# Optimization experiments

Measured on AMD Instinct MI355X. Metric: run time of the kernel, lower is better.

Reference implementation:

```python
import jax, jax.numpy as jnp
import numpy as np

N_NODES = 100000
N_EDGES = 800000
N_GRAPHS = 256
IN_C = 96
HID = 96
OUT_C = 16


def setup_inputs() -> dict:
    key = jax.random.key(0)
    ks = jax.random.split(key, 10)
    x = jax.random.normal(ks[0], (N_NODES, IN_C), dtype=jnp.float32)
    edge_index = jax.random.randint(ks[1], (2, N_EDGES), 0, N_NODES, dtype=jnp.int64)
    batch = jnp.sort(jax.random.randint(ks[2], (N_NODES,), 0, N_GRAPHS, dtype=jnp.int64))
    def glorot(k, fan_in, fan_out):
        s = np.sqrt(6.0 / (fan_in + fan_out)).astype(np.float32)
        return jax.random.uniform(k, (fan_in, fan_out), minval=-s, maxval=s, dtype=jnp.float32)
    W1 = glorot(ks[3], IN_C, HID)
    W2 = glorot(ks[4], HID, HID)
    W3 = glorot(ks[5], HID, HID)
    Wlin = glorot(ks[6], HID, OUT_C)
    b1 = jnp.zeros((HID,), dtype=jnp.float32)
    b2 = jnp.zeros((HID,), dtype=jnp.float32)
    b3 = jnp.zeros((HID,), dtype=jnp.float32)
    return {"x": x, "edge_index": edge_index, "batch": batch,
            "W1": W1, "b1": b1, "W2": W2, "b2": b2, "W3": W3, "b3": b3, "Wlin": Wlin}


def _gcn_conv(x, W, b, src, dst):
    # PyG GCNConv(normalize=True): add self-loops, deg includes self-loop,
    # norm_ij = deg_i^{-1/2} * deg_j^{-1/2}; linear (no bias) then scatter-add; bias after.
    n = x.shape[0]
    deg = jnp.zeros((n,), dtype=x.dtype).at[dst].add(1.0) + 1.0  # +1 self-loop
    dinv = jax.lax.rsqrt(deg)
    h = x @ W                                   # [N, H]
    coef = dinv[src] * dinv[dst]                # [E]
    msg = h[src] * coef[:, None]                # [E, H] gather
    agg = jax.ops.segment_sum(msg, dst, num_segments=n)  # scatter-add
    agg = agg + h * (dinv * dinv)[:, None]      # self-loop contribution
    return agg + b


def reference(x, edge_index, batch, W1, b1, W2, b2, W3, b3, Wlin):
    src, dst = edge_index[0], edge_index[1]
    h = jax.nn.relu(_gcn_conv(x, W1, b1, src, dst))
    h = jax.nn.relu(_gcn_conv(h, W2, b2, src, dst))
    h = _gcn_conv(h, W3, b3, src, dst)
    # global mean pool over graphs
    sums = jax.ops.segment_sum(h, batch, num_segments=N_GRAPHS)
    counts = jax.ops.segment_sum(jnp.ones((h.shape[0],), dtype=h.dtype), batch, num_segments=N_GRAPHS)
    pooled = sums / jnp.maximum(counts, 1.0)[:, None]
    return pooled @ Wlin
```

## Files before the change

### kernel.cpp

```cpp
#include <hip/hip_runtime.h>

#define NN 100000
#define NE 800000
#define NG 256
#define CH 96
#define OC 16
#define NBLK 391
#define TM 128

typedef __attribute__((ext_vector_type(8))) short bf16x8;
typedef __attribute__((ext_vector_type(4))) float f32x4;

__device__ __forceinline__ unsigned short f2bf(float x) {
    unsigned u = __float_as_uint(x);
    return (unsigned short)((u + 0x7fffu + ((u >> 16) & 1u)) >> 16);
}
__device__ __forceinline__ float bf2f(unsigned short h) {
    return __uint_as_float(((unsigned)h) << 16);
}
__device__ __forceinline__ void split8(const float4 a, const float4 b,
                                       bf16x8& hi, bf16x8& lo) {
    float v[8] = {a.x, a.y, a.z, a.w, b.x, b.y, b.z, b.w};
#pragma unroll
    for (int j = 0; j < 8; j++) {
        unsigned short h = f2bf(v[j]);
        hi[j] = (short)h;
        lo[j] = (short)f2bf(v[j] - bf2f(h));
    }
}
__device__ __forceinline__ float4 us4_to_f4(ushort4 u) {
    return make_float4(bf2f(u.x), bf2f(u.y), bf2f(u.z), bf2f(u.w));
}

__global__ __launch_bounds__(256) void k_hist(const int* __restrict__ dst,
                                              int* __restrict__ cnt,
                                              int* __restrict__ slot) {
    int e = blockIdx.x * 256 + threadIdx.x;
    slot[e] = atomicAdd(&cnt[dst[e]], 1);
}

__global__ __launch_bounds__(256) void k_offsets(const int* __restrict__ cnt,
                                                 int* __restrict__ gtot,
                                                 int* __restrict__ off,
                                                 float* __restrict__ dinv,
                                                 const int* __restrict__ batch,
                                                 int* __restrict__ goff) {
    int i = blockIdx.x * 256 + threadIdx.x;
    if (i >= NN) return;
    int c = cnt[i];
    off[i] = atomicAdd(gtot, c);
    dinv[i] = rsqrtf((float)c + 1.0f);
    int b = batch[i];
    int bp = (i > 0) ? batch[i - 1] : -1;
    for (int g = bp + 1; g <= b; g++) goff[g] = i;
    if (i == NN - 1)
        for (int g = b + 1; g <= NG; g++) goff[g] = NN;
}

__global__ __launch_bounds__(256) void k_build(const int* __restrict__ src,
                                               const int* __restrict__ dst,
                                               const int* __restrict__ off,
                                               const int* __restrict__ slot,
                                               const float* __restrict__ dinv,
                                               float2* __restrict__ packed) {
    int e = blockIdx.x * 256 + threadIdx.x;
    int s = src[e];
    int d = dst[e];
    packed[off[d] + slot[e]] = make_float2(__int_as_float(s), dinv[s] * dinv[d]);
    if (blockIdx.x == 0 && threadIdx.x < 8)
        packed[NE + threadIdx.x] = make_float2(__int_as_float(0), 0.0f);
}

__global__ __launch_bounds__(256) void k_prep(const float* __restrict__ W1,
                                              const float* __restrict__ W2,
                                              const float* __restrict__ W3,
                                              unsigned short* __restrict__ WH,
                                              unsigned short* __restrict__ WL) {
    int id = blockIdx.x * 256 + threadIdx.x;
    if (id >= 3 * CH * CH) return;
    int w = id / (CH * CH);
    int r = id - w * CH * CH;
    int k = r / CH;
    int n = r - k * CH;
    const float* Ws = (w == 0) ? W1 : (w == 1) ? W2 : W3;
    float v = Ws[k * CH + n];
    unsigned short h = f2bf(v);
    WH[w * CH * CH + n * CH + k] = h;
    WL[w * CH * CH + n * CH + k] = f2bf(v - bf2f(h));
}

__global__ __launch_bounds__(256) void k_gemm96(const float* __restrict__ X,
                                                const unsigned short* __restrict__ WH,
                                                const unsigned short* __restrict__ WL,
                                                unsigned short* __restrict__ H) {
    __shared__ __align__(16) unsigned short WsH[CH * CH];
    __shared__ __align__(16) unsigned short WsL[CH * CH];

    const int tid = threadIdx.x;
    const int n0 = blockIdx.x * TM;

    {
        const uint4* sH = reinterpret_cast<const uint4*>(WH);
        const uint4* sL = reinterpret_cast<const uint4*>(WL);
        uint4* dH = reinterpret_cast<uint4*>(WsH);
        uint4* dL = reinterpret_cast<uint4*>(WsL);
        for (int i = tid; i < CH * CH / 8; i += 256) {
            dH[i] = sH[i];
            dL[i] = sL[i];
        }
    }
    __syncthreads();

    const int lane = tid & 63;
    const int wave = tid >> 6;
    const int lrow = lane & 15;
    const int quad = lane >> 4;

    const float4* X4 = reinterpret_cast<const float4*>(X);

    f32x4 acc[2][6];
#pragma unroll
    for (int rt = 0; rt < 2; rt++)
#pragma unroll
        for (int ct = 0; ct < 6; ct++) acc[rt][ct] = (f32x4){0.f, 0.f, 0.f, 0.f};

    int arow[2];
#pragma unroll
    for (int rt = 0; rt < 2; rt++)
        arow[rt] = min(n0 + (wave * 2 + rt) * 16 + lrow, NN - 1);

#pragma unroll
    for (int kc = 0; kc < 3; kc++) {
        bf16x8 ahi[2], alo[2];
#pragma unroll
        for (int rt = 0; rt < 2; rt++) {
            int fo = (arow[rt] * CH + kc * 32 + quad * 8) >> 2;
            split8(X4[fo], X4[fo + 1], ahi[rt], alo[rt]);
        }
#pragma unroll
        for (int ct = 0; ct < 6; ct++) {
            int bo = (ct * 16 + lrow) * CH + kc * 32 + quad * 8;
            bf16x8 bhi = *reinterpret_cast<const bf16x8*>(&WsH[bo]);
            bf16x8 blo = *reinterpret_cast<const bf16x8*>(&WsL[bo]);
#pragma unroll
            for (int rt = 0; rt < 2; rt++) {
                acc[rt][ct] = __builtin_amdgcn_mfma_f32_16x16x32_bf16(
                    alo[rt], bhi, acc[rt][ct], 0, 0, 0);
                acc[rt][ct] = __builtin_amdgcn_mfma_f32_16x16x32_bf16(
                    ahi[rt], blo, acc[rt][ct], 0, 0, 0);
                acc[rt][ct] = __builtin_amdgcn_mfma_f32_16x16x32_bf16(
                    ahi[rt], bhi, acc[rt][ct], 0, 0, 0);
            }
        }
    }

#pragma unroll
    for (int rt = 0; rt < 2; rt++) {
        int rbase = n0 + (wave * 2 + rt) * 16 + quad * 4;
#pragma unroll
        for (int ct = 0; ct < 6; ct++) {
            int col = ct * 16 + lrow;
#pragma unroll
            for (int r = 0; r < 4; r++) {
                int row = rbase + r;
                if (row < NN) H[(size_t)row * CH + col] = f2bf(acc[rt][ct][r]);
            }
        }
    }
}

template <bool RELU>
__global__ __launch_bounds__(256) void k_aggregate(const int* __restrict__ off,
                                                   const int* __restrict__ cnt,
                                                   const float2* __restrict__ packed,
                                                   const float* __restrict__ dinv,
                                                   const float* __restrict__ bias,
                                                   const unsigned short* __restrict__ H,
                                                   float* __restrict__ B) {
    int idx = blockIdx.x * 256 + threadIdx.x;
    int n = idx / 24;
    int c4 = idx - n * 24;
    int e0 = off[n];
    int e1 = e0 + cnt[n];

    const ushort4* H4 = reinterpret_cast<const ushort4*>(H);
    float di = dinv[n];
    float d2 = di * di;
    float4 h = us4_to_f4(H4[(size_t)n * 24 + c4]);
    float4 bb = reinterpret_cast<const float4*>(bias)[c4];
    float4 acc = make_float4(h.x * d2 + bb.x, h.y * d2 + bb.y,
                             h.z * d2 + bb.z, h.w * d2 + bb.w);

    for (int e = e0; e < e1; e += 4) {
        float2 p0 = packed[e + 0];
        float2 p1 = packed[e + 1];
        float2 p2 = packed[e + 2];
        float2 p3 = packed[e + 3];
        float c0 = p0.y;
        float c1 = (e + 1 < e1) ? p1.y : 0.0f;
        float c2 = (e + 2 < e1) ? p2.y : 0.0f;
        float c3 = (e + 3 < e1) ? p3.y : 0.0f;
        float4 v0 = us4_to_f4(H4[(size_t)__float_as_int(p0.x) * 24 + c4]);
        float4 v1 = us4_to_f4(H4[(size_t)__float_as_int(p1.x) * 24 + c4]);
        float4 v2 = us4_to_f4(H4[(size_t)__float_as_int(p2.x) * 24 + c4]);
        float4 v3 = us4_to_f4(H4[(size_t)__float_as_int(p3.x) * 24 + c4]);
        acc.x += v0.x * c0 + v1.x * c1 + v2.x * c2 + v3.x * c3;
        acc.y += v0.y * c0 + v1.y * c1 + v2.y * c2 + v3.y * c3;
        acc.z += v0.z * c0 + v1.z * c1 + v2.z * c2 + v3.z * c3;
        acc.w += v0.w * c0 + v1.w * c1 + v2.w * c2 + v3.w * c3;
    }
    if (RELU) {
        acc.x = fmaxf(acc.x, 0.0f); acc.y = fmaxf(acc.y, 0.0f);
        acc.z = fmaxf(acc.z, 0.0f); acc.w = fmaxf(acc.w, 0.0f);
    }
    reinterpret_cast<float4*>(B)[(size_t)n * 24 + c4] = acc;
}


__global__ __launch_bounds__(384) void k_pool_linear(const int* __restrict__ goff,
                                                     const float* __restrict__ B,
                                                     const float* __restrict__ Wlin,
                                                     float* __restrict__ out) {
    __shared__ float4 sh[16][24];
    __shared__ float pooled[CH];
    int g = blockIdx.x;
    int t = threadIdx.x;
    int nl = t / 24;
    int c4 = t - nl * 24;
    int s = goff[g];
    int e = goff[g + 1];

    float4 acc = make_float4(0.f, 0.f, 0.f, 0.f);
    const float4* B4 = reinterpret_cast<const float4*>(B);
    for (int n = s + nl; n < e; n += 16) {
        float4 v = B4[(size_t)n * 24 + c4];
        acc.x += v.x; acc.y += v.y; acc.z += v.z; acc.w += v.w;
    }
    sh[nl][c4] = acc;
    __syncthreads();

    if (t < 24) {
        float4 r = make_float4(0.f, 0.f, 0.f, 0.f);
#pragma unroll
        for (int j = 0; j < 16; j++) {
            float4 v = sh[j][t];
            r.x += v.x; r.y += v.y; r.z += v.z; r.w += v.w;
        }
        float inv = 1.0f / fmaxf((float)(e - s), 1.0f);
        pooled[t * 4 + 0] = r.x * inv;
        pooled[t * 4 + 1] = r.y * inv;
        pooled[t * 4 + 2] = r.z * inv;
        pooled[t * 4 + 3] = r.w * inv;
    }
    __syncthreads();

    if (t < OC) {
        float a = 0.0f;
#pragma unroll 8
        for (int k = 0; k < CH; k++) a += pooled[k] * Wlin[k * OC + t];
        out[g * OC + t] = a;
    }
}

extern "C" void kernel_launch(void* const* d_in, const int* in_sizes, int n_in,
                              void* d_out, int out_size, void* d_ws, size_t ws_size,
                              hipStream_t stream) {
    const float* x = (const float*)d_in[0];
    const int* ei = (const int*)d_in[1];
    const int* src = ei;
    const int* dst = ei + NE;
    const int* batch = (const int*)d_in[2];
    const float* W1 = (const float*)d_in[3];
    const float* b1 = (const float*)d_in[4];
    const float* W2 = (const float*)d_in[5];
    const float* b2 = (const float*)d_in[6];
    const float* W3 = (const float*)d_in[7];
    const float* b3 = (const float*)d_in[8];
    const float* Wlin = (const float*)d_in[9];
    float* out = (float*)d_out;

    char* ws = (char*)d_ws;
    unsigned short* Ha = (unsigned short*)ws;  ws += (size_t)NN * CH * 2;
    unsigned short* Hb = (unsigned short*)ws;  ws += (size_t)NN * CH * 2;
    float* B = (float*)ws;          ws += (size_t)NN * CH * 4;
    float2* packed = (float2*)ws;   ws += (size_t)(NE + 8) * 8;
    unsigned short* WH = (unsigned short*)ws;  ws += 3 * CH * CH * 2;
    unsigned short* WL = (unsigned short*)ws;  ws += 3 * CH * CH * 2;
    float* dinv = (float*)ws;       ws += NN * 4;
    int* off = (int*)ws;            ws += NN * 4;
    int* goff = (int*)ws;           ws += 272 * 4;
    int* cnt = (int*)ws;            ws += (NN + 4) * 4;
    int* gtot = cnt + NN;
    int* slot = (int*)B;

    hipMemsetAsync(cnt, 0, (NN + 4) * 4, stream);
    k_hist<<<NE / 256, 256, 0, stream>>>(dst, cnt, slot);
    k_offsets<<<NBLK, 256, 0, stream>>>(cnt, gtot, off, dinv, batch, goff);
    k_build<<<NE / 256, 256, 0, stream>>>(src, dst, off, slot, dinv, packed);
    k_prep<<<(3 * CH * CH + 255) / 256, 256, 0, stream>>>(W1, W2, W3, WH, WL);

    const int gblk = (NN + TM - 1) / TM;

    k_gemm96<<<gblk, 256, 0, stream>>>(x, WH, WL, Ha);
    k_aggregate<true><<<NN * 24 / 256, 256, 0, stream>>>(off, cnt, packed, dinv, b1, Ha, B);

    k_gemm96<<<gblk, 256, 0, stream>>>(B, WH + CH * CH, WL + CH * CH, Hb);
    k_aggregate<true><<<NN * 24 / 256, 256, 0, stream>>>(off, cnt, packed, dinv, b2, Hb, B);

    k_gemm96<<<gblk, 256, 0, stream>>>(B, WH + 2 * CH * CH, WL + 2 * CH * CH, Ha);
    k_aggregate<false><<<NN * 24 / 256, 256, 0, stream>>>(off, cnt, packed, dinv, b3, Ha, B);

    k_pool_linear<<<NG, 384, 0, stream>>>(goff, B, Wlin, out);
}
```

Measured before the change: 331.3 us.

## Store intermediate layer activations in bf16 and fold weight prep into histogram

```diff
diff --git a/kernel.cpp b/kernel.cpp
--- a/kernel.cpp
+++ b/kernel.cpp
@@ -34,9 +34,25 @@
 
 __global__ __launch_bounds__(256) void k_hist(const int* __restrict__ dst,
                                               int* __restrict__ cnt,
-                                              int* __restrict__ slot) {
+                                              int* __restrict__ slot,
+                                              const float* __restrict__ W1,
+                                              const float* __restrict__ W2,
+                                              const float* __restrict__ W3,
+                                              unsigned short* __restrict__ WH,
+                                              unsigned short* __restrict__ WL) {
     int e = blockIdx.x * 256 + threadIdx.x;
     slot[e] = atomicAdd(&cnt[dst[e]], 1);
+    if (e < 3 * CH * CH) {
+        int w = e / (CH * CH);
+        int r = e - w * (CH * CH);
+        int k = r / CH;
+        int n = r - k * CH;
+        const float* Ws = (w == 0) ? W1 : (w == 1) ? W2 : W3;
+        float v = Ws[k * CH + n];
+        unsigned short h = f2bf(v);
+        WH[w * CH * CH + n * CH + k] = h;
+        WL[w * CH * CH + n * CH + k] = f2bf(v - bf2f(h));
+    }
 }
 
 __global__ __launch_bounds__(256) void k_offsets(const int* __restrict__ cnt,
@@ -67,32 +83,12 @@
     int s = src[e];
     int d = dst[e];
     packed[off[d] + slot[e]] = make_float2(__int_as_float(s), dinv[s] * dinv[d]);
-    if (blockIdx.x == 0 && threadIdx.x < 8)
-        packed[NE + threadIdx.x] = make_float2(__int_as_float(0), 0.0f);
-}
-
-__global__ __launch_bounds__(256) void k_prep(const float* __restrict__ W1,
-                                              const float* __restrict__ W2,
-                                              const float* __restrict__ W3,
-                                              unsigned short* __restrict__ WH,
-                                              unsigned short* __restrict__ WL) {
-    int id = blockIdx.x * 256 + threadIdx.x;
-    if (id >= 3 * CH * CH) return;
-    int w = id / (CH * CH);
-    int r = id - w * CH * CH;
-    int k = r / CH;
-    int n = r - k * CH;
-    const float* Ws = (w == 0) ? W1 : (w == 1) ? W2 : W3;
-    float v = Ws[k * CH + n];
-    unsigned short h = f2bf(v);
-    WH[w * CH * CH + n * CH + k] = h;
-    WL[w * CH * CH + n * CH + k] = f2bf(v - bf2f(h));
-}
-
-__global__ __launch_bounds__(256) void k_gemm96(const float* __restrict__ X,
-                                                const unsigned short* __restrict__ WH,
-                                                const unsigned short* __restrict__ WL,
-                                                unsigned short* __restrict__ H) {
+}
+
+__global__ __launch_bounds__(256) void k_gemm_f32(const float* __restrict__ X,
+                                                  const unsigned short* __restrict__ WH,
+                                                  const unsigned short* __restrict__ WL,
+                                                  unsigned short* __restrict__ H) {
     __shared__ __align__(16) unsigned short WsH[CH * CH];
     __shared__ __align__(16) unsigned short WsL[CH * CH];
 
@@ -169,14 +165,89 @@
     }
 }
 
-template <bool RELU>
+__global__ __launch_bounds__(256) void k_gemm_bf16(const unsigned short* __restrict__ X,
+                                                   const unsigned short* __restrict__ WH,
+                                                   const unsigned short* __restrict__ WL,
+                                                   unsigned short* __restrict__ H) {
+    __shared__ __align__(16) unsigned short WsH[CH * CH];
+    __shared__ __align__(16) unsigned short WsL[CH * CH];
+
+    const int tid = threadIdx.x;
+    const int n0 = blockIdx.x * TM;
+
+    {
+        const uint4* sH = reinterpret_cast<const uint4*>(WH);
+        const uint4* sL = reinterpret_cast<const uint4*>(WL);
+        uint4* dH = reinterpret_cast<uint4*>(WsH);
+        uint4* dL = reinterpret_cast<uint4*>(WsL);
+        for (int i = tid; i < CH * CH / 8; i += 256) {
+            dH[i] = sH[i];
+            dL[i] = sL[i];
+        }
+    }
+    __syncthreads();
+
+    const int lane = tid & 63;
+    const int wave = tid >> 6;
+    const int lrow = lane & 15;
+    const int quad = lane >> 4;
+
+    f32x4 acc[2][6];
+#pragma unroll
+    for (int rt = 0; rt < 2; rt++)
+#pragma unroll
+        for (int ct = 0; ct < 6; ct++) acc[rt][ct] = (f32x4){0.f, 0.f, 0.f, 0.f};
+
+    int arow[2];
+#pragma unroll
+    for (int rt = 0; rt < 2; rt++)
+        arow[rt] = min(n0 + (wave * 2 + rt) * 16 + lrow, NN - 1);
+
+#pragma unroll
+    for (int kc = 0; kc < 3; kc++) {
+        bf16x8 ahi[2];
+#pragma unroll
+        for (int rt = 0; rt < 2; rt++)
+            ahi[rt] = *reinterpret_cast<const bf16x8*>(
+                &X[(size_t)arow[rt] * CH + kc * 32 + quad * 8]);
+#pragma unroll
+        for (int ct = 0; ct < 6; ct++) {
+            int bo = (ct * 16 + lrow) * CH + kc * 32 + quad * 8;
+            bf16x8 bhi = *reinterpret_cast<const bf16x8*>(&WsH[bo]);
+            bf16x8 blo = *reinterpret_cast<const bf16x8*>(&WsL[bo]);
+#pragma unroll
+            for (int rt = 0; rt < 2; rt++) {
+                acc[rt][ct] = __builtin_amdgcn_mfma_f32_16x16x32_bf16(
+                    ahi[rt], blo, acc[rt][ct], 0, 0, 0);
+                acc[rt][ct] = __builtin_amdgcn_mfma_f32_16x16x32_bf16(
+                    ahi[rt], bhi, acc[rt][ct], 0, 0, 0);
+            }
+        }
+    }
+
+#pragma unroll
+    for (int rt = 0; rt < 2; rt++) {
+        int rbase = n0 + (wave * 2 + rt) * 16 + quad * 4;
+#pragma unroll
+        for (int ct = 0; ct < 6; ct++) {
+            int col = ct * 16 + lrow;
+#pragma unroll
+            for (int r = 0; r < 4; r++) {
+                int row = rbase + r;
+                if (row < NN) H[(size_t)row * CH + col] = f2bf(acc[rt][ct][r]);
+            }
+        }
+    }
+}
+
+template <bool RELU, bool B16OUT>
 __global__ __launch_bounds__(256) void k_aggregate(const int* __restrict__ off,
                                                    const int* __restrict__ cnt,
                                                    const float2* __restrict__ packed,
                                                    const float* __restrict__ dinv,
                                                    const float* __restrict__ bias,
                                                    const unsigned short* __restrict__ H,
-                                                   float* __restrict__ B) {
+                                                   void* __restrict__ Bout) {
     int idx = blockIdx.x * 256 + threadIdx.x;
     int n = idx / 24;
     int c4 = idx - n * 24;
@@ -191,31 +262,39 @@
     float4 acc = make_float4(h.x * d2 + bb.x, h.y * d2 + bb.y,
                              h.z * d2 + bb.z, h.w * d2 + bb.w);
 
-    for (int e = e0; e < e1; e += 4) {
+    int e = e0;
+    for (; e + 4 <= e1; e += 4) {
         float2 p0 = packed[e + 0];
         float2 p1 = packed[e + 1];
         float2 p2 = packed[e + 2];
         float2 p3 = packed[e + 3];
-        float c0 = p0.y;
-        float c1 = (e + 1 < e1) ? p1.y : 0.0f;
-        float c2 = (e + 2 < e1) ? p2.y : 0.0f;
-        float c3 = (e + 3 < e1) ? p3.y : 0.0f;
         float4 v0 = us4_to_f4(H4[(size_t)__float_as_int(p0.x) * 24 + c4]);
         float4 v1 = us4_to_f4(H4[(size_t)__float_as_int(p1.x) * 24 + c4]);
         float4 v2 = us4_to_f4(H4[(size_t)__float_as_int(p2.x) * 24 + c4]);
         float4 v3 = us4_to_f4(H4[(size_t)__float_as_int(p3.x) * 24 + c4]);
-        acc.x += v0.x * c0 + v1.x * c1 + v2.x * c2 + v3.x * c3;
-        acc.y += v0.y * c0 + v1.y * c1 + v2.y * c2 + v3.y * c3;
-        acc.z += v0.z * c0 + v1.z * c1 + v2.z * c2 + v3.z * c3;
-        acc.w += v0.w * c0 + v1.w * c1 + v2.w * c2 + v3.w * c3;
+        acc.x += v0.x * p0.y + v1.x * p1.y + v2.x * p2.y + v3.x * p3.y;
+        acc.y += v0.y * p0.y + v1.y * p1.y + v2.y * p2.y + v3.y * p3.y;
+        acc.z += v0.z * p0.y + v1.z * p1.y + v2.z * p2.y + v3.z * p3.y;
+        acc.w += v0.w * p0.y + v1.w * p1.y + v2.w * p2.y + v3.w * p3.y;
+    }
+    for (; e < e1; e++) {
+        float2 pc = packed[e];
+        float4 v = us4_to_f4(H4[(size_t)__float_as_int(pc.x) * 24 + c4]);
+        acc.x += v.x * pc.y; acc.y += v.y * pc.y;
+        acc.z += v.z * pc.y; acc.w += v.w * pc.y;
     }
     if (RELU) {
         acc.x = fmaxf(acc.x, 0.0f); acc.y = fmaxf(acc.y, 0.0f);
         acc.z = fmaxf(acc.z, 0.0f); acc.w = fmaxf(acc.w, 0.0f);
     }
-    reinterpret_cast<float4*>(B)[(size_t)n * 24 + c4] = acc;
-}
-
+    if (B16OUT) {
+        ushort4 o;
+        o.x = f2bf(acc.x); o.y = f2bf(acc.y); o.z = f2bf(acc.z); o.w = f2bf(acc.w);
+        reinterpret_cast<ushort4*>(Bout)[(size_t)n * 24 + c4] = o;
+    } else {
+        reinterpret_cast<float4*>(Bout)[(size_t)n * 24 + c4] = acc;
+    }
+}
 
 __global__ __launch_bounds__(384) void k_pool_linear(const int* __restrict__ goff,
                                                      const float* __restrict__ B,
@@ -282,8 +361,9 @@
     char* ws = (char*)d_ws;
     unsigned short* Ha = (unsigned short*)ws;  ws += (size_t)NN * CH * 2;
     unsigned short* Hb = (unsigned short*)ws;  ws += (size_t)NN * CH * 2;
+    unsigned short* Bb = (unsigned short*)ws;  ws += (size_t)NN * CH * 2;
     float* B = (float*)ws;          ws += (size_t)NN * CH * 4;
-    float2* packed = (float2*)ws;   ws += (size_t)(NE + 8) * 8;
+    float2* packed = (float2*)ws;   ws += (size_t)NE * 8;
     unsigned short* WH = (unsigned short*)ws;  ws += 3 * CH * CH * 2;
     unsigned short* WL = (unsigned short*)ws;  ws += 3 * CH * CH * 2;
     float* dinv = (float*)ws;       ws += NN * 4;
@@ -294,21 +374,23 @@
     int* slot = (int*)B;
 
     hipMemsetAsync(cnt, 0, (NN + 4) * 4, stream);
-    k_hist<<<NE / 256, 256, 0, stream>>>(dst, cnt, slot);
+    k_hist<<<NE / 256, 256, 0, stream>>>(dst, cnt, slot, W1, W2, W3, WH, WL);
     k_offsets<<<NBLK, 256, 0, stream>>>(cnt, gtot, off, dinv, batch, goff);
     k_build<<<NE / 256, 256, 0, stream>>>(src, dst, off, slot, dinv, packed);
-    k_prep<<<(3 * CH * CH + 255) / 256, 256, 0, stream>>>(W1, W2, W3, WH, WL);
 
     const int gblk = (NN + TM - 1) / TM;
 
-    k_gemm96<<<gblk, 256, 0, stream>>>(x, WH, WL, Ha);
-    k_aggregate<true><<<NN * 24 / 256, 256, 0, stream>>>(off, cnt, packed, dinv, b1, Ha, B);
-
-    k_gemm96<<<gblk, 256, 0, stream>>>(B, WH + CH * CH, WL + CH * CH, Hb);
-    k_aggregate<true><<<NN * 24 / 256, 256, 0, stream>>>(off, cnt, packed, dinv, b2, Hb, B);
-
-    k_gemm96<<<gblk, 256, 0, stream>>>(B, WH + 2 * CH * CH, WL + 2 * CH * CH, Ha);
-    k_aggregate<false><<<NN * 24 / 256, 256, 0, stream>>>(off, cnt, packed, dinv, b3, Ha, B);
+    k_gemm_f32<<<gblk, 256, 0, stream>>>(x, WH, WL, Ha);
+    k_aggregate<true, true><<<NN * 24 / 256, 256, 0, stream>>>(
+        off, cnt, packed, dinv, b1, Ha, Bb);
+
+    k_gemm_bf16<<<gblk, 256, 0, stream>>>(Bb, WH + CH * CH, WL + CH * CH, Hb);
+    k_aggregate<true, true><<<NN * 24 / 256, 256, 0, stream>>>(
+        off, cnt, packed, dinv, b2, Hb, Bb);
+
+    k_gemm_bf16<<<gblk, 256, 0, stream>>>(Bb, WH + 2 * CH * CH, WL + 2 * CH * CH, Ha);
+    k_aggregate<false, false><<<NN * 24 / 256, 256, 0, stream>>>(
+        off, cnt, packed, dinv, b3, Ha, B);
 
     k_pool_linear<<<NG, 384, 0, stream>>>(goff, B, Wlin, out);
 }
```

Measured after the change: 323.4 us. 2.4% less time.
